# Kernel optimization log

Hardware: AMD Instinct MI355X
Metric: run time of the kernel (lower is better)

The kernel has to match this reference:

```python
import jax, jax.numpy as jnp
import numpy as np

B, H, S, D = 2, 16, 2048, 64

def setup_inputs() -> dict:
    key0 = jax.random.key(0)
    kq, kk, kv = jax.random.split(key0, 3)
    return {
        "query": jax.random.normal(kq, (B, H, S, D), dtype=jnp.float32),
        "key": jax.random.normal(kk, (B, H, S, D), dtype=jnp.float32),
        "value": jax.random.normal(kv, (B, H, S, D), dtype=jnp.float32),
        "inv_scale_factor": jnp.full((1,), np.sqrt(D), dtype=jnp.float32),
    }

def reference(query, key, value, inv_scale_factor):
    # qk: [B,H,S,S]
    qk = jnp.einsum("bhqd,bhkd->bhqk", query, key)
    scaled_qk = qk / inv_scale_factor
    softmax_qk = jax.nn.softmax(scaled_qk, axis=-1)
    # dropout_p = 0.0 -> identity (deterministic reference)
    out = jnp.einsum("bhqk,bhkd->bhqd", softmax_qk, value)
    return out
```

## Files before the change

kernel.cpp:

```cpp
#include <hip/hip_runtime.h>
#include <hip/hip_bf16.h>


typedef __attribute__((ext_vector_type(8))) short short8;
typedef __attribute__((ext_vector_type(4))) float floatx4;

#define NB 2
#define NH 16
#define SS 2048
#define DD 64

#define QM 64
#define KN 64
#define KSTR 72
#define VSTR 72
#define PSTR 72
#define OSTR 68
#define NITER (SS / KN)

#define MSHIFT 9.0f
#define LOG2E 1.44269504f

#define MFMA16(a, b, c) __builtin_amdgcn_mfma_f32_16x16x32_bf16(a, b, c, 0, 0, 0)
#define WAIT_LGKM0() __builtin_amdgcn_s_waitcnt(0x007F)

static __device__ inline unsigned pack2bf(float a, float b) {
    unsigned ua = __builtin_bit_cast(unsigned, a) + 0x8000u;
    unsigned ub = __builtin_bit_cast(unsigned, b) + 0x8000u;
    return __builtin_amdgcn_perm(ub, ua, 0x07060302u);
}

__global__ __launch_bounds__(256, 4)
void fattn_kernel(const float* __restrict__ Q, const float* __restrict__ K,
                  const float* __restrict__ V, const float* __restrict__ isf,
                  float* __restrict__ O)
{
    __shared__ __align__(16) char smem[27648];
    short* K_lds  = (short*)smem;
    short* Vt_lds = (short*)(smem + 9216);
    short* P_lds  = (short*)(smem + 18432);
    float* O_buf  = (float*)smem;
    float* l_buf  = (float*)(smem + 17408);

    const int tid  = threadIdx.x;
    const int wave = tid >> 6;
    const int w_m  = wave & 1;
    const int w_n  = wave >> 1;
    const int lane = tid & 63;
    const int l15  = lane & 15;
    const int quad = lane >> 4;

    const int b    = blockIdx.x & 1023;
    const int xcd  = b & 7;
    const int j    = b >> 3;
    const int head = xcd + 8 * (j & 3);
    const int qt   = j >> 2;

    const float scl2 = (1.0f / isf[0]) * LOG2E;
    const float msh2 = MSHIFT * LOG2E;

    const size_t hoff = (size_t)head * SS * DD;
    const float* Qh = Q + hoff;
    const float* Kh = K + hoff;
    const float* Vh = V + hoff;
    float*       Oh = O + hoff;

    short8 q_frag[2][2];
#pragma unroll
    for (int mt = 0; mt < 2; ++mt) {
        const float* qrow = Qh + (size_t)(qt * QM + w_m * 32 + mt * 16 + l15) * DD;
#pragma unroll
        for (int ks = 0; ks < 2; ++ks) {
            float4 f0 = *(const float4*)(qrow + ks * 32 + quad * 8);
            float4 f1 = *(const float4*)(qrow + ks * 32 + quad * 8 + 4);
            uint4 qp;
            qp.x = pack2bf(f0.x, f0.y);
            qp.y = pack2bf(f0.z, f0.w);
            qp.z = pack2bf(f1.x, f1.y);
            qp.w = pack2bf(f1.z, f1.w);
            q_frag[mt][ks] = __builtin_bit_cast(short8, qp);
        }
    }

    floatx4 o_acc[2][4];
#pragma unroll
    for (int mt = 0; mt < 2; ++mt)
#pragma unroll
        for (int dt = 0; dt < 4; ++dt)
#pragma unroll
            for (int i = 0; i < 4; ++i) o_acc[mt][dt][i] = 0.0f;

    float lsum[2] = {0.0f, 0.0f};

    const int vd = tid & 63;
    const int vg = tid >> 6;

    float4 kpre[4];
    float  vpre[16];
#pragma unroll
    for (int k = 0; k < 4; ++k)
        kpre[k] = *(const float4*)(Kh + (size_t)(k * 256 + tid) * 4);
    {
        const float* Vsrc = Vh + (size_t)(vg * 16) * DD + vd;
#pragma unroll
        for (int jj = 0; jj < 16; ++jj) vpre[jj] = Vsrc[jj * DD];
    }

    for (int kb = 0; kb < NITER; ++kb) {
#pragma unroll
        for (int k = 0; k < 4; ++k) {
            int f4 = k * 256 + tid;
            int r  = f4 >> 4;
            int c  = (f4 & 15) * 4;
            uint2 pk;
            pk.x = pack2bf(kpre[k].x, kpre[k].y);
            pk.y = pack2bf(kpre[k].z, kpre[k].w);
            *(uint2*)&K_lds[r * KSTR + c] = pk;
        }
        {
            uint4 lo, hi;
            lo.x = pack2bf(vpre[0],  vpre[1]);
            lo.y = pack2bf(vpre[2],  vpre[3]);
            lo.z = pack2bf(vpre[4],  vpre[5]);
            lo.w = pack2bf(vpre[6],  vpre[7]);
            hi.x = pack2bf(vpre[8],  vpre[9]);
            hi.y = pack2bf(vpre[10], vpre[11]);
            hi.z = pack2bf(vpre[12], vpre[13]);
            hi.w = pack2bf(vpre[14], vpre[15]);
            *(uint4*)&Vt_lds[vd * VSTR + vg * 16]     = lo;
            *(uint4*)&Vt_lds[vd * VSTR + vg * 16 + 8] = hi;
        }
        __syncthreads();

        {
            int nxt = (kb + 1 < NITER) ? kb + 1 : kb;
            const float* Ksrc = Kh + (size_t)nxt * KN * DD;
#pragma unroll
            for (int k = 0; k < 4; ++k)
                kpre[k] = *(const float4*)(Ksrc + (size_t)(k * 256 + tid) * 4);
            const float* Vsrc = Vh + (size_t)(nxt * KN + vg * 16) * DD + vd;
#pragma unroll
            for (int jj = 0; jj < 16; ++jj) vpre[jj] = Vsrc[jj * DD];
        }

        floatx4 s[2][2];
#pragma unroll
        for (int mt = 0; mt < 2; ++mt)
#pragma unroll
            for (int nt = 0; nt < 2; ++nt)
#pragma unroll
                for (int i = 0; i < 4; ++i) s[mt][nt][i] = 0.0f;
#pragma unroll
        for (int ks = 0; ks < 2; ++ks)
#pragma unroll
            for (int nt = 0; nt < 2; ++nt) {
                short8 a = *(short8*)&K_lds[(w_n * 32 + nt * 16 + l15) * KSTR + ks * 32 + quad * 8];
                s[0][nt] = MFMA16(a, q_frag[0][ks], s[0][nt]);
                s[1][nt] = MFMA16(a, q_frag[1][ks], s[1][nt]);
            }

#pragma unroll
        for (int mt = 0; mt < 2; ++mt) {
            const int prow = (w_m * 32 + mt * 16 + l15) * PSTR + w_n * 32;
#pragma unroll
            for (int nt = 0; nt < 2; ++nt) {
                float p0 = exp2f(fmaf(s[mt][nt][0], scl2, -msh2));
                float p1 = exp2f(fmaf(s[mt][nt][1], scl2, -msh2));
                float p2 = exp2f(fmaf(s[mt][nt][2], scl2, -msh2));
                float p3 = exp2f(fmaf(s[mt][nt][3], scl2, -msh2));
                lsum[mt] += (p0 + p1) + (p2 + p3);
                uint2 pk;
                pk.x = pack2bf(p0, p1);
                pk.y = pack2bf(p2, p3);
                *(uint2*)&P_lds[prow + nt * 16 + quad * 4] = pk;
            }
        }

        WAIT_LGKM0();

        short8 pf[2];
#pragma unroll
        for (int mt = 0; mt < 2; ++mt)
            pf[mt] = *(short8*)&P_lds[(w_m * 32 + mt * 16 + l15) * PSTR + w_n * 32 + quad * 8];
#pragma unroll
        for (int dt = 0; dt < 4; ++dt) {
            short8 vf = *(short8*)&Vt_lds[(dt * 16 + l15) * VSTR + w_n * 32 + quad * 8];
            o_acc[0][dt] = MFMA16(vf, pf[0], o_acc[0][dt]);
            o_acc[1][dt] = MFMA16(vf, pf[1], o_acc[1][dt]);
        }
        __syncthreads();
    }

#pragma unroll
    for (int mt = 0; mt < 2; ++mt) {
        lsum[mt] += __shfl_xor(lsum[mt], 16);
        lsum[mt] += __shfl_xor(lsum[mt], 32);
    }
    __syncthreads();

    if (w_n == 1) {
#pragma unroll
        for (int mt = 0; mt < 2; ++mt) {
            const int orow = (w_m * 32 + mt * 16 + l15) * OSTR;
#pragma unroll
            for (int dt = 0; dt < 4; ++dt) {
                float4 v = { o_acc[mt][dt][0], o_acc[mt][dt][1],
                             o_acc[mt][dt][2], o_acc[mt][dt][3] };
                *(float4*)&O_buf[orow + dt * 16 + quad * 4] = v;
            }
            if (quad == 0) l_buf[w_m * 32 + mt * 16 + l15] = lsum[mt];
        }
    }
    __syncthreads();
    if (w_n == 0) {
#pragma unroll
        for (int mt = 0; mt < 2; ++mt) {
            const int m_blk = w_m * 32 + mt * 16 + l15;
            float lt = lsum[mt] + l_buf[m_blk];
            float rl = 1.0f / lt;
            float* orow = Oh + (size_t)(qt * QM + m_blk) * DD;
#pragma unroll
            for (int dt = 0; dt < 4; ++dt) {
                float4 part = *(float4*)&O_buf[m_blk * OSTR + dt * 16 + quad * 4];
                float4 v;
                v.x = (o_acc[mt][dt][0] + part.x) * rl;
                v.y = (o_acc[mt][dt][1] + part.y) * rl;
                v.z = (o_acc[mt][dt][2] + part.z) * rl;
                v.w = (o_acc[mt][dt][3] + part.w) * rl;
                *(float4*)(orow + dt * 16 + quad * 4) = v;
            }
        }
    }
}

extern "C" void kernel_launch(void* const* d_in, const int* in_sizes, int n_in,
                              void* d_out, int out_size, void* d_ws, size_t ws_size,
                              hipStream_t stream) {
    const float* Q   = (const float*)d_in[0];
    const float* K   = (const float*)d_in[1];
    const float* V   = (const float*)d_in[2];
    const float* isf = (const float*)d_in[3];
    float* O = (float*)d_out;
    const int n_heads = NB * NH;
    const int n_qt    = SS / QM;
    fattn_kernel<<<n_heads * n_qt, 256, 0, stream>>>(Q, K, V, isf, O);
}
```

Before: 164.9 us.

## Double-buffer K/V in LDS with XOR swizzle and one barrier per iteration

K and V tiles now live in two LDS buffers. The next tile is packed and stored into the alternate buffer after the PV MFMAs, which removes the trailing __syncthreads so each key block needs only one barrier. Padded row strides are replaced by an XOR swizzle on 8-element groups for K, V and P, to avoid LDS bank conflicts without padding. K global loads are reorganised so each thread stores 16-byte vectors. Shared memory per block grows from about 27 KB to 40 KB, which may limit occupancy at 4 blocks per CU.

```diff
diff --git a/kernel.cpp b/kernel.cpp
--- a/kernel.cpp
+++ b/kernel.cpp
@@ -12,10 +12,6 @@
 
 #define QM 64
 #define KN 64
-#define KSTR 72
-#define VSTR 72
-#define PSTR 72
-#define OSTR 68
 #define NITER (SS / KN)
 
 #define MSHIFT 9.0f
@@ -28,6 +24,10 @@
     unsigned ua = __builtin_bit_cast(unsigned, a) + 0x8000u;
     unsigned ub = __builtin_bit_cast(unsigned, b) + 0x8000u;
     return __builtin_amdgcn_perm(ub, ua, 0x07060302u);
+}
+
+static __device__ inline int swz(int row, int col) {
+    return row * 64 + ((((col >> 3) ^ row) & 7) << 3) + (col & 7);
 }
 
 __global__ __launch_bounds__(256, 4)
@@ -35,12 +35,13 @@
                   const float* __restrict__ V, const float* __restrict__ isf,
                   float* __restrict__ O)
 {
-    __shared__ __align__(16) char smem[27648];
-    short* K_lds  = (short*)smem;
-    short* Vt_lds = (short*)(smem + 9216);
-    short* P_lds  = (short*)(smem + 18432);
-    float* O_buf  = (float*)smem;
-    float* l_buf  = (float*)(smem + 17408);
+    __shared__ __align__(16) char smem[40960];
+    short* Kbuf  = (short*)smem;
+    short* Vbuf  = (short*)(smem + 16384);
+    short* P_lds = (short*)(smem + 32768);
+    float* O_buf = (float*)smem;
+    float* l_buf = (float*)(smem + 17408);
+#define OSTR 68
 
     const int tid  = threadIdx.x;
     const int wave = tid >> 6;
@@ -92,52 +93,59 @@
 
     float lsum[2] = {0.0f, 0.0f};
 
+    const int kr = tid >> 3;
+    const int kc = tid & 7;
     const int vd = tid & 63;
     const int vg = tid >> 6;
 
     float4 kpre[4];
     float  vpre[16];
-#pragma unroll
-    for (int k = 0; k < 4; ++k)
-        kpre[k] = *(const float4*)(Kh + (size_t)(k * 256 + tid) * 4);
+
+#pragma unroll
+    for (int x = 0; x < 2; ++x) {
+        const float* src = Kh + (size_t)(x * 32 + kr) * DD + kc * 8;
+        kpre[2 * x]     = *(const float4*)src;
+        kpre[2 * x + 1] = *(const float4*)(src + 4);
+    }
     {
         const float* Vsrc = Vh + (size_t)(vg * 16) * DD + vd;
 #pragma unroll
         for (int jj = 0; jj < 16; ++jj) vpre[jj] = Vsrc[jj * DD];
     }
+#pragma unroll
+    for (int x = 0; x < 2; ++x) {
+        int r = x * 32 + kr;
+        uint4 w;
+        w.x = pack2bf(kpre[2 * x].x,     kpre[2 * x].y);
+        w.y = pack2bf(kpre[2 * x].z,     kpre[2 * x].w);
+        w.z = pack2bf(kpre[2 * x + 1].x, kpre[2 * x + 1].y);
+        w.w = pack2bf(kpre[2 * x + 1].z, kpre[2 * x + 1].w);
+        *(uint4*)&Kbuf[swz(r, kc * 8)] = w;
+    }
+    {
+        uint4 lo, hi;
+        lo.x = pack2bf(vpre[0],  vpre[1]);  lo.y = pack2bf(vpre[2],  vpre[3]);
+        lo.z = pack2bf(vpre[4],  vpre[5]);  lo.w = pack2bf(vpre[6],  vpre[7]);
+        hi.x = pack2bf(vpre[8],  vpre[9]);  hi.y = pack2bf(vpre[10], vpre[11]);
+        hi.z = pack2bf(vpre[12], vpre[13]); hi.w = pack2bf(vpre[14], vpre[15]);
+        *(uint4*)&Vbuf[swz(vd, vg * 16)]     = lo;
+        *(uint4*)&Vbuf[swz(vd, vg * 16 + 8)] = hi;
+    }
 
     for (int kb = 0; kb < NITER; ++kb) {
-#pragma unroll
-        for (int k = 0; k < 4; ++k) {
-            int f4 = k * 256 + tid;
-            int r  = f4 >> 4;
-            int c  = (f4 & 15) * 4;
-            uint2 pk;
-            pk.x = pack2bf(kpre[k].x, kpre[k].y);
-            pk.y = pack2bf(kpre[k].z, kpre[k].w);
-            *(uint2*)&K_lds[r * KSTR + c] = pk;
-        }
-        {
-            uint4 lo, hi;
-            lo.x = pack2bf(vpre[0],  vpre[1]);
-            lo.y = pack2bf(vpre[2],  vpre[3]);
-            lo.z = pack2bf(vpre[4],  vpre[5]);
-            lo.w = pack2bf(vpre[6],  vpre[7]);
-            hi.x = pack2bf(vpre[8],  vpre[9]);
-            hi.y = pack2bf(vpre[10], vpre[11]);
-            hi.z = pack2bf(vpre[12], vpre[13]);
-            hi.w = pack2bf(vpre[14], vpre[15]);
-            *(uint4*)&Vt_lds[vd * VSTR + vg * 16]     = lo;
-            *(uint4*)&Vt_lds[vd * VSTR + vg * 16 + 8] = hi;
-        }
         __syncthreads();
+        const short* Kb = Kbuf + (kb & 1) * 4096;
+        const short* Vb = Vbuf + (kb & 1) * 4096;
 
         {
             int nxt = (kb + 1 < NITER) ? kb + 1 : kb;
             const float* Ksrc = Kh + (size_t)nxt * KN * DD;
 #pragma unroll
-            for (int k = 0; k < 4; ++k)
-                kpre[k] = *(const float4*)(Ksrc + (size_t)(k * 256 + tid) * 4);
+            for (int x = 0; x < 2; ++x) {
+                const float* src = Ksrc + (size_t)(x * 32 + kr) * DD + kc * 8;
+                kpre[2 * x]     = *(const float4*)src;
+                kpre[2 * x + 1] = *(const float4*)(src + 4);
+            }
             const float* Vsrc = Vh + (size_t)(nxt * KN + vg * 16) * DD + vd;
 #pragma unroll
             for (int jj = 0; jj < 16; ++jj) vpre[jj] = Vsrc[jj * DD];
@@ -154,14 +162,14 @@
         for (int ks = 0; ks < 2; ++ks)
 #pragma unroll
             for (int nt = 0; nt < 2; ++nt) {
-                short8 a = *(short8*)&K_lds[(w_n * 32 + nt * 16 + l15) * KSTR + ks * 32 + quad * 8];
+                short8 a = *(const short8*)&Kb[swz(w_n * 32 + nt * 16 + l15, ks * 32 + quad * 8)];
                 s[0][nt] = MFMA16(a, q_frag[0][ks], s[0][nt]);
                 s[1][nt] = MFMA16(a, q_frag[1][ks], s[1][nt]);
             }
 
 #pragma unroll
         for (int mt = 0; mt < 2; ++mt) {
-            const int prow = (w_m * 32 + mt * 16 + l15) * PSTR + w_n * 32;
+            const int m = w_m * 32 + mt * 16 + l15;
 #pragma unroll
             for (int nt = 0; nt < 2; ++nt) {
                 float p0 = exp2f(fmaf(s[mt][nt][0], scl2, -msh2));
@@ -172,7 +180,7 @@
                 uint2 pk;
                 pk.x = pack2bf(p0, p1);
                 pk.y = pack2bf(p2, p3);
-                *(uint2*)&P_lds[prow + nt * 16 + quad * 4] = pk;
+                *(uint2*)&P_lds[swz(m, w_n * 32 + nt * 16 + quad * 4)] = pk;
             }
         }
 
@@ -181,14 +189,35 @@
         short8 pf[2];
 #pragma unroll
         for (int mt = 0; mt < 2; ++mt)
-            pf[mt] = *(short8*)&P_lds[(w_m * 32 + mt * 16 + l15) * PSTR + w_n * 32 + quad * 8];
+            pf[mt] = *(const short8*)&P_lds[swz(w_m * 32 + mt * 16 + l15, w_n * 32 + quad * 8)];
 #pragma unroll
         for (int dt = 0; dt < 4; ++dt) {
-            short8 vf = *(short8*)&Vt_lds[(dt * 16 + l15) * VSTR + w_n * 32 + quad * 8];
+            short8 vf = *(const short8*)&Vb[swz(dt * 16 + l15, w_n * 32 + quad * 8)];
             o_acc[0][dt] = MFMA16(vf, pf[0], o_acc[0][dt]);
             o_acc[1][dt] = MFMA16(vf, pf[1], o_acc[1][dt]);
         }
-        __syncthreads();
+
+        {
+            short* Kn = Kbuf + ((kb + 1) & 1) * 4096;
+            short* Vn = Vbuf + ((kb + 1) & 1) * 4096;
+#pragma unroll
+            for (int x = 0; x < 2; ++x) {
+                int r = x * 32 + kr;
+                uint4 w;
+                w.x = pack2bf(kpre[2 * x].x,     kpre[2 * x].y);
+                w.y = pack2bf(kpre[2 * x].z,     kpre[2 * x].w);
+                w.z = pack2bf(kpre[2 * x + 1].x, kpre[2 * x + 1].y);
+                w.w = pack2bf(kpre[2 * x + 1].z, kpre[2 * x + 1].w);
+                *(uint4*)&Kn[swz(r, kc * 8)] = w;
+            }
+            uint4 lo, hi;
+            lo.x = pack2bf(vpre[0],  vpre[1]);  lo.y = pack2bf(vpre[2],  vpre[3]);
+            lo.z = pack2bf(vpre[4],  vpre[5]);  lo.w = pack2bf(vpre[6],  vpre[7]);
+            hi.x = pack2bf(vpre[8],  vpre[9]);  hi.y = pack2bf(vpre[10], vpre[11]);
+            hi.z = pack2bf(vpre[12], vpre[13]); hi.w = pack2bf(vpre[14], vpre[15]);
+            *(uint4*)&Vn[swz(vd, vg * 16)]     = lo;
+            *(uint4*)&Vn[swz(vd, vg * 16 + 8)] = hi;
+        }
     }
 
 #pragma unroll
```

Result: slower. 171.1 us (+3.7%).
